# Performance work log

Hardware: AMD Instinct MI355X
Metric: run time of the kernel (lower is better)

The kernel has to match this reference:

```python
import jax, jax.numpy as jnp
import numpy as np

N_NODES = 20000
N_EDGES = 320000
IN_DIM = 128
HID = 256
HEADS = 8
DH = HID // HEADS  # 32
LAYERS = 3
NUM_GRAPHS = 64
OUT_DIM = 10
SLOPE = 0.2  # DGL GATv2Conv default negative_slope


def setup_inputs() -> dict:
    key = jax.random.key(0)
    ks = jax.random.split(key, 20)
    s_in = 1.0 / np.sqrt(IN_DIM)
    s_h = 1.0 / np.sqrt(HID)
    s_h2 = 1.0 / np.sqrt(HID // 2)
    return {
        "feature": jax.random.normal(ks[0], (N_NODES, IN_DIM), jnp.float32),
        "W_in": jax.random.normal(ks[1], (IN_DIM, HID), jnp.float32) * s_in,
        "b_in": jax.random.normal(ks[2], (HID,), jnp.float32) * 0.01,
        "W_src": jax.random.normal(ks[3], (LAYERS, HID, HID), jnp.float32) * s_h,
        "b_src": jax.random.normal(ks[4], (LAYERS, HID), jnp.float32) * 0.01,
        "W_dst": jax.random.normal(ks[5], (LAYERS, HID, HID), jnp.float32) * s_h,
        "b_dst": jax.random.normal(ks[6], (LAYERS, HID), jnp.float32) * 0.01,
        "attn": jax.random.normal(ks[7], (LAYERS, HEADS, DH), jnp.float32) * (1.0 / np.sqrt(DH)),
        "Wc1": jax.random.normal(ks[8], (HID, HID), jnp.float32) * s_h,
        "bc1": jax.random.normal(ks[9], (HID,), jnp.float32) * 0.01,
        "Wc2": jax.random.normal(ks[10], (HID, HID // 2), jnp.float32) * s_h,
        "bc2": jax.random.normal(ks[11], (HID // 2,), jnp.float32) * 0.01,
        "Wc3": jax.random.normal(ks[12], (HID // 2, OUT_DIM), jnp.float32) * s_h2,
        "bc3": jax.random.normal(ks[13], (OUT_DIM,), jnp.float32) * 0.01,
        "src": jax.random.randint(ks[14], (N_EDGES,), 0, N_NODES, jnp.int32),
        "dst": jax.random.randint(ks[15], (N_EDGES,), 0, N_NODES, jnp.int32),
        "graph_ids": jnp.sort(jax.random.randint(ks[16], (N_NODES,), 0, NUM_GRAPHS, jnp.int32)),
    }


def _gatv2_layer(h, Ws, bs, Wd, bd, a, src, dst):
    # DGL GATv2Conv: e_ij = a^T LeakyReLU(W_src h_j + W_dst h_i), edge softmax over
    # incoming edges of dst, scatter-sum of alpha * W_src h_src; residual = Identity
    # (in_feats == heads*out_feats); activation relu.
    n = h.shape[0]
    fs = (h @ Ws + bs).reshape(n, HEADS, DH)  # [N,H,D]
    fd = (h @ Wd + bd).reshape(n, HEADS, DH)
    e = jax.nn.leaky_relu(fs[src] + fd[dst], SLOPE)          # [E,H,D]
    score = jnp.einsum("ehd,hd->eh", e, a)                   # [E,H]
    m = jax.ops.segment_max(score, dst, num_segments=n)       # stable softmax max
    ex = jnp.exp(score - m[dst])
    denom = jax.ops.segment_sum(ex, dst, num_segments=n)
    alpha = ex / denom[dst]                                    # [E,H]
    rst = jax.ops.segment_sum(alpha[:, :, None] * fs[src], dst, num_segments=n)
    out = jax.nn.relu(rst + h.reshape(n, HEADS, DH))          # residual + activation
    return out.reshape(n, HID)


def reference(feature, W_in, b_in, W_src, b_src, W_dst, b_dst, attn,
              Wc1, bc1, Wc2, bc2, Wc3, bc3, src, dst, graph_ids):
    h = feature @ W_in + b_in
    for l in range(LAYERS):
        h = _gatv2_layer(h, W_src[l], b_src[l], W_dst[l], b_dst[l], attn[l], src, dst)
    # dgl.sum_nodes over batched graph -> per-graph segment sum
    hg = jax.ops.segment_sum(h, graph_ids, num_segments=NUM_GRAPHS)  # [G,HID]
    # classifier (dropout is identity in eval mode)
    x = jax.nn.relu(hg @ Wc1 + bc1)
    x = jax.nn.relu(x @ Wc2 + bc2)
    return x @ Wc3 + bc3  # [G,OUT_DIM]
```

## Files before the change

### kernel.cpp

```cpp
#include <hip/hip_runtime.h>
#include <hip/hip_bf16.h>
#include <math.h>

#define N_NODES 20000
#define N_EDGES 320000
#define IN_DIM 128
#define HID 256
#define HEADS 8
#define DH 32
#define LAYERS 3
#define NUM_GRAPHS 64
#define OUT_DIM 10
#define SLOPE 0.2f

#define NBKT 5
#define N_BINS (N_NODES * NBKT)
#define SCAN_BLK 1024
#define SCAN_NBLK ((N_BINS + SCAN_BLK - 1) / SCAN_BLK)

typedef __bf16 bf16x8 __attribute__((ext_vector_type(8)));
typedef float f32x4 __attribute__((ext_vector_type(4)));

static __device__ __forceinline__ unsigned short f2bfbits(float v) {
    __bf16 b = (__bf16)v;
    return __builtin_bit_cast(unsigned short, b);
}
static __device__ __forceinline__ void unpack8(uint4 u, float* f) {
    unsigned p0 = u.x, p1 = u.y, p2 = u.z, p3 = u.w;
    f[0] = __builtin_bit_cast(float, p0 << 16);
    f[1] = __builtin_bit_cast(float, p0 & 0xffff0000u);
    f[2] = __builtin_bit_cast(float, p1 << 16);
    f[3] = __builtin_bit_cast(float, p1 & 0xffff0000u);
    f[4] = __builtin_bit_cast(float, p2 << 16);
    f[5] = __builtin_bit_cast(float, p2 & 0xffff0000u);
    f[6] = __builtin_bit_cast(float, p3 << 16);
    f[7] = __builtin_bit_cast(float, p3 & 0xffff0000u);
}
static __device__ __forceinline__ void unpack4(uint2 u, float* f) {
    f[0] = __builtin_bit_cast(float, u.x << 16);
    f[1] = __builtin_bit_cast(float, u.x & 0xffff0000u);
    f[2] = __builtin_bit_cast(float, u.y << 16);
    f[3] = __builtin_bit_cast(float, u.y & 0xffff0000u);
}

typedef const __attribute__((address_space(1))) unsigned int* as1_u32p;
typedef __attribute__((address_space(3))) unsigned int* as3_u32p;
static __device__ __forceinline__ void async_cp16(const unsigned short* g, unsigned short* l) {
    __builtin_amdgcn_global_load_lds((as1_u32p)g, (as3_u32p)l, 16, 0, 0);
}

#define CAST_N4 (N_NODES * IN_DIM / 4)
#define WTRANS_TOTAL (IN_DIM * HID + 6 * HID * HID)
#define ZERO_TOTAL (N_BINS + NUM_GRAPHS * HID)
#define PREP_TOTAL (CAST_N4 + WTRANS_TOTAL + ZERO_TOTAL)
__global__ void prep_kernel(const float* __restrict__ feat,
                            const float* __restrict__ Win,
                            const float* __restrict__ Wsrc,
                            const float* __restrict__ Wdst,
                            unsigned short* __restrict__ featH,
                            unsigned short* __restrict__ WinT,
                            unsigned short* __restrict__ WT,
                            int* __restrict__ cnt, float* __restrict__ hg) {
    int idx = blockIdx.x * blockDim.x + threadIdx.x;
    if (idx < CAST_N4) {
        float4 v = ((const float4*)feat)[idx];
        ushort4 o;
        o.x = f2bfbits(v.x); o.y = f2bfbits(v.y);
        o.z = f2bfbits(v.z); o.w = f2bfbits(v.w);
        ((ushort4*)featH)[idx] = o;
    } else if (idx < CAST_N4 + WTRANS_TOTAL) {
        int j = idx - CAST_N4;
        if (j < IN_DIM * HID) {
            int n = j / IN_DIM, k = j % IN_DIM;
            WinT[j] = f2bfbits(Win[k * HID + n]);
        } else {
            int r6 = j - IN_DIM * HID;
            int mat = r6 >> 16;
            int r = r6 & 65535;
            int n = r >> 8, k = r & 255;
            const float* base = (mat < 3) ? (Wsrc + (size_t)mat * 65536)
                                          : (Wdst + (size_t)(mat - 3) * 65536);
            WT[r6] = f2bfbits(base[k * 256 + n]);
        }
    } else if (idx < PREP_TOTAL) {
        int z = idx - CAST_N4 - WTRANS_TOTAL;
        if (z < N_BINS) cnt[z] = 0;
        else hg[z - N_BINS] = 0.f;
    }
}

__global__ void count_kernel(const int* __restrict__ src, const int* __restrict__ dst,
                             int* __restrict__ cnt) {
    int e = blockIdx.x * blockDim.x + threadIdx.x;
    if (e < N_EDGES) atomicAdd(&cnt[dst[e] * NBKT + (src[e] >> 12)], 1);
}

__global__ __launch_bounds__(1024) void scan_partial(const int* __restrict__ cnt,
                                                     int* __restrict__ bsum) {
    __shared__ int wsum[16];
    int t = threadIdx.x;
    int idx = blockIdx.x * SCAN_BLK + t;
    int x = (idx < N_BINS) ? cnt[idx] : 0;
    int v = x;
#pragma unroll
    for (int d = 1; d < 64; d <<= 1) v += __shfl_xor(v, d, 64);
    if ((t & 63) == 0) wsum[t >> 6] = v;
    __syncthreads();
    if (t == 0) {
        int s = 0;
#pragma unroll
        for (int i = 0; i < 16; ++i) s += wsum[i];
        bsum[blockIdx.x] = s;
    }
}

__global__ __launch_bounds__(1024) void scan_scatter(const int* __restrict__ cnt,
                                                     const int* __restrict__ bsum,
                                                     int* __restrict__ offs,
                                                     int* __restrict__ cursor) {
    __shared__ int wsum[16];
    __shared__ int bpart[128];
    __shared__ int sbase;
    int t = threadIdx.x;
    int blk = blockIdx.x;
    if (t < 128) bpart[t] = (t < blk) ? bsum[t] : 0;
    __syncthreads();
    if (t < 64) {
        int r = bpart[t] + bpart[t + 64];
#pragma unroll
        for (int d = 1; d < 64; d <<= 1) r += __shfl_xor(r, d, 64);
        if (t == 0) sbase = r;
    }
    int idx = blk * SCAN_BLK + t;
    int x = (idx < N_BINS) ? cnt[idx] : 0;
    int v = x;
#pragma unroll
    for (int d = 1; d < 64; d <<= 1) {
        int u = __shfl_up(v, d, 64);
        if ((t & 63) >= d) v += u;
    }
    if ((t & 63) == 63) wsum[t >> 6] = v;
    __syncthreads();
    if (t < 16) {
        int wv = wsum[t];
#pragma unroll
        for (int d = 1; d < 16; d <<= 1) {
            int u = __shfl_up(wv, d, 64);
            if (t >= d) wv += u;
        }
        wsum[t] = wv;
    }
    __syncthreads();
    int waveoff = (t >> 6) ? wsum[(t >> 6) - 1] : 0;
    int ex = sbase + waveoff + v - x;
    if (idx < N_BINS) { offs[idx] = ex; cursor[idx] = ex; }
    if (blk == SCAN_NBLK - 1 && t == SCAN_BLK - 1) offs[N_BINS] = ex + x;
}

__global__ void fill_kernel(const int* __restrict__ src, const int* __restrict__ dst,
                            int* __restrict__ cursor, int* __restrict__ csr_src) {
    int e = blockIdx.x * blockDim.x + threadIdx.x;
    if (e < N_EDGES) {
        int sv = src[e];
        int p = atomicAdd(&cursor[dst[e] * NBKT + (sv >> 12)], 1);
        csr_src[p] = sv;
    }
}

template <int DUAL>
__global__ __launch_bounds__(256, 4) void mfma_gemm(
    const unsigned short* __restrict__ Ah,
    const unsigned short* __restrict__ BT1, const float* __restrict__ bias1,
    unsigned short* __restrict__ O1,
    const unsigned short* __restrict__ BT2, const float* __restrict__ bias2,
    unsigned short* __restrict__ O2,
    int M, int K, int N) {
    __shared__ __align__(16) unsigned short As[2][64 * 32];
    __shared__ __align__(16) unsigned short Bs1[2][128 * 32];
    __shared__ __align__(16) unsigned short Bs2[DUAL ? 2 : 1][DUAL ? 128 * 32 : 8];

    const int t = threadIdx.x;
    const int wv = t >> 6, lane = t & 63, quad = lane >> 4, l15 = lane & 15;
    const int m0 = blockIdx.x * 64, n0 = blockIdx.y * 128;

    const int sA = wv * 64 + lane;
    const int rA = sA >> 2, cA = (sA & 3) ^ ((rA >> 1) & 3);
    int gmA = m0 + rA; if (gmA >= M) gmA = M - 1;
    const size_t offA = (size_t)gmA * K + cA * 8;
    const int sB0 = wv * 64 + lane, sB1v = sB0 + 256;
    const int rB0 = sB0 >> 2, cB0 = (sB0 & 3) ^ ((rB0 >> 1) & 3);
    const int rB1 = sB1v >> 2, cB1 = (sB1v & 3) ^ ((rB1 >> 1) & 3);
    const size_t offB0 = (size_t)(n0 + rB0) * K + cB0 * 8;
    const size_t offB1 = (size_t)(n0 + rB1) * K + cB1 * 8;

    auto issue = [&](int buf, int k0) {
        async_cp16(Ah + offA + k0, &As[buf][wv * 512]);
        async_cp16(BT1 + offB0 + k0, &Bs1[buf][wv * 512]);
        async_cp16(BT1 + offB1 + k0, &Bs1[buf][2048 + wv * 512]);
        if (DUAL) {
            async_cp16(BT2 + offB0 + k0, &Bs2[buf][wv * 512]);
            async_cp16(BT2 + offB1 + k0, &Bs2[buf][2048 + wv * 512]);
        }
    };

    const int mrow0 = (wv >> 1) * 32;
    const int ncb = (wv & 1) * 64;

    f32x4 zero = {0.f, 0.f, 0.f, 0.f};
    f32x4 acc1[2][4], acc2[2][4];
#pragma unroll
    for (int mi = 0; mi < 2; ++mi)
#pragma unroll
        for (int t4 = 0; t4 < 4; ++t4) { acc1[mi][t4] = zero; acc2[mi][t4] = zero; }

    issue(0, 0);
    int buf = 0;
    for (int k0 = 0; k0 < K; k0 += 32, buf ^= 1) {
        __syncthreads();
        if (k0 + 32 < K) issue(buf ^ 1, k0 + 32);

        bf16x8 aF[2];
#pragma unroll
        for (int mi = 0; mi < 2; ++mi) {
            int row = mrow0 + mi * 16 + l15;
            int aoff = row * 32 + ((quad ^ ((row >> 1) & 3)) << 3);
            aF[mi] = __builtin_bit_cast(bf16x8, *(const uint4*)(&As[buf][0] + aoff));
        }
#pragma unroll
        for (int t4 = 0; t4 < 4; ++t4) {
            int brow = ncb + t4 * 16 + l15;
            int boff = brow * 32 + ((quad ^ ((brow >> 1) & 3)) << 3);
            bf16x8 b1 = __builtin_bit_cast(bf16x8, *(const uint4*)(&Bs1[buf][0] + boff));
#pragma unroll
            for (int mi = 0; mi < 2; ++mi)
                acc1[mi][t4] = __builtin_amdgcn_mfma_f32_16x16x32_bf16(aF[mi], b1, acc1[mi][t4], 0, 0, 0);
            if (DUAL) {
                bf16x8 b2 = __builtin_bit_cast(bf16x8, *(const uint4*)(&Bs2[buf][0] + boff));
#pragma unroll
                for (int mi = 0; mi < 2; ++mi)
                    acc2[mi][t4] = __builtin_amdgcn_mfma_f32_16x16x32_bf16(aF[mi], b2, acc2[mi][t4], 0, 0, 0);
            }
        }
    }

    float bia1[4], bia2[4];
#pragma unroll
    for (int t4 = 0; t4 < 4; ++t4) {
        bia1[t4] = bias1[n0 + ncb + t4 * 16 + l15];
        bia2[t4] = DUAL ? bias2[n0 + ncb + t4 * 16 + l15] : 0.f;
    }
#pragma unroll
    for (int mi = 0; mi < 2; ++mi) {
#pragma unroll
        for (int t4 = 0; t4 < 4; ++t4) {
            int gn = n0 + ncb + t4 * 16 + l15;
#pragma unroll
            for (int r = 0; r < 4; ++r) {
                int gm = m0 + mrow0 + mi * 16 + quad * 4 + r;
                if (gm < M) {
                    float v = acc1[mi][t4][r] + bia1[t4];
                    O1[(size_t)gm * N + gn] = f2bfbits(v);
                    if (DUAL) {
                        float v2 = acc2[mi][t4][r] + bia2[t4];
                        O2[(size_t)gm * N + gn] = f2bfbits(v2);
                    }
                }
            }
        }
    }
}

__global__ __launch_bounds__(256) void gat_agg2(
    const unsigned short* __restrict__ fsb, const unsigned short* __restrict__ fdb,
    unsigned short* __restrict__ hb, const int* __restrict__ offs,
    const int* __restrict__ csr_src, const float* __restrict__ attn_l) {
    int tid = threadIdx.x;
    int node = (blockIdx.x * blockDim.x + tid) >> 5;
    if (node >= N_NODES) return;
    int l32 = tid & 31;
    int dbase = l32 * 8;
    int abase = (l32 >> 2) * DH + (l32 & 3) * 8;

    float a[8];
#pragma unroll
    for (int j = 0; j < 8; ++j) a[j] = attn_l[abase + j];

    float fdv[8];
    unpack8(*(const uint4*)(fdb + (size_t)node * HID + dbase), fdv);

    float ssum0 = 0.f, ssum1 = 0.f;
    float acc0[8], acc1[8];
#pragma unroll
    for (int j = 0; j < 8; ++j) { acc0[j] = 0.f; acc1[j] = 0.f; }

    auto procE = [&](uint4 u, float* acc, float& ssum) {
        float fsv[8];
        unpack8(u, fsv);
        float p = 0.f;
#pragma unroll
        for (int j = 0; j < 8; ++j) {
            float e = fsv[j] + fdv[j];
            e = fmaxf(e, SLOPE * e);
            p += e * a[j];
        }
        p += __shfl_xor(p, 1, 64);
        p += __shfl_xor(p, 2, 64);
        float w = __expf(p);
        ssum += w;
#pragma unroll
        for (int j = 0; j < 8; ++j) acc[j] += w * fsv[j];
    };

    const unsigned short* fsl = fsb + dbase;
    int beg = offs[node * NBKT], end = offs[node * NBKT + NBKT];
    int nfull = (end - beg) >> 2;
    const int limit = beg + nfull * 4;

    uint4 cu0, cu1, cu2, cu3;
    int ci0, ci1, ci2, ci3;
    int base = beg + 8;
    bool have = (nfull >= 1);
    bool haveN = (nfull >= 2);
    if (have) {
        int s0 = csr_src[beg], s1 = csr_src[beg + 1];
        int s2 = csr_src[beg + 2], s3 = csr_src[beg + 3];
        if (haveN) {
            ci0 = csr_src[beg + 4]; ci1 = csr_src[beg + 5];
            ci2 = csr_src[beg + 6]; ci3 = csr_src[beg + 7];
        }
        cu0 = *(const uint4*)(fsl + (size_t)s0 * HID);
        cu1 = *(const uint4*)(fsl + (size_t)s1 * HID);
        cu2 = *(const uint4*)(fsl + (size_t)s2 * HID);
        cu3 = *(const uint4*)(fsl + (size_t)s3 * HID);
    }
    while (have) {
        uint4 nu0, nu1, nu2, nu3;
        int ni0, ni1, ni2, ni3;
        if (haveN) {
            nu0 = *(const uint4*)(fsl + (size_t)ci0 * HID);
            nu1 = *(const uint4*)(fsl + (size_t)ci1 * HID);
            nu2 = *(const uint4*)(fsl + (size_t)ci2 * HID);
            nu3 = *(const uint4*)(fsl + (size_t)ci3 * HID);
        }
        bool haveNN = (base + 4 <= limit);
        if (haveNN) {
            ni0 = csr_src[base]; ni1 = csr_src[base + 1];
            ni2 = csr_src[base + 2]; ni3 = csr_src[base + 3];
        }
        base += 4;
        procE(cu0, acc0, ssum0);
        procE(cu1, acc1, ssum1);
        procE(cu2, acc0, ssum0);
        procE(cu3, acc1, ssum1);
        if (haveN) { cu0 = nu0; cu1 = nu1; cu2 = nu2; cu3 = nu3; }
        if (haveNN) { ci0 = ni0; ci1 = ni1; ci2 = ni2; ci3 = ni3; }
        have = haveN; haveN = haveNN;
    }
    for (int idx = limit; idx < end; ++idx) {
        int sv = csr_src[idx];
        procE(*(const uint4*)(fsl + (size_t)sv * HID), acc0, ssum0);
    }

    float ssum = ssum0 + ssum1;
    float acc[8];
#pragma unroll
    for (int j = 0; j < 8; ++j) acc[j] = acc0[j] + acc1[j];

    float inv = ssum > 0.f ? 1.f / ssum : 0.f;
    float hv[8];
    unpack8(*(const uint4*)(hb + (size_t)node * HID + dbase), hv);
    unsigned short ob[8];
#pragma unroll
    for (int j = 0; j < 8; ++j) {
        float o = fmaxf(acc[j] * inv + hv[j], 0.f);
        ob[j] = f2bfbits(o);
    }
    *(uint4*)(hb + (size_t)node * HID + dbase) = *(uint4*)ob;
}

#define POOL_CHUNK 32
__global__ __launch_bounds__(64) void pool_kernel(const unsigned short* __restrict__ hb,
                                                  const int* __restrict__ gid,
                                                  float* __restrict__ hg) {
    int t = threadIdx.x;
    int n0 = blockIdx.x * POOL_CHUNK;
    int n1 = n0 + POOL_CHUNK; if (n1 > N_NODES) n1 = N_NODES;
    if (n0 >= N_NODES) return;
    float acc[4] = {0.f, 0.f, 0.f, 0.f};
    int cur = gid[n0];
    for (int n = n0; n < n1; ++n) {
        int g = gid[n];
        if (g != cur) {
            atomicAdd(&hg[(size_t)cur * HID + t * 4 + 0], acc[0]);
            atomicAdd(&hg[(size_t)cur * HID + t * 4 + 1], acc[1]);
            atomicAdd(&hg[(size_t)cur * HID + t * 4 + 2], acc[2]);
            atomicAdd(&hg[(size_t)cur * HID + t * 4 + 3], acc[3]);
            acc[0] = acc[1] = acc[2] = acc[3] = 0.f;
            cur = g;
        }
        float v[4];
        unpack4(*(const uint2*)(hb + (size_t)n * HID + t * 4), v);
        acc[0] += v[0]; acc[1] += v[1]; acc[2] += v[2]; acc[3] += v[3];
    }
    atomicAdd(&hg[(size_t)cur * HID + t * 4 + 0], acc[0]);
    atomicAdd(&hg[(size_t)cur * HID + t * 4 + 1], acc[1]);
    atomicAdd(&hg[(size_t)cur * HID + t * 4 + 2], acc[2]);
    atomicAdd(&hg[(size_t)cur * HID + t * 4 + 3], acc[3]);
}

__global__ __launch_bounds__(256) void classifier_kernel(
    const float* __restrict__ hg,
    const float* __restrict__ Wc1, const float* __restrict__ bc1,
    const float* __restrict__ Wc2, const float* __restrict__ bc2,
    const float* __restrict__ Wc3, const float* __restrict__ bc3,
    float* __restrict__ out) {
    __shared__ float xin[HID];
    __shared__ float x1[HID];
    __shared__ float x2[HID / 2];
    int g = blockIdx.x, t = threadIdx.x;
    xin[t] = hg[(size_t)g * HID + t];
    __syncthreads();
    {
        float acc = bc1[t];
        for (int k = 0; k < HID; ++k) acc += xin[k] * Wc1[k * HID + t];
        x1[t] = fmaxf(acc, 0.f);
    }
    __syncthreads();
    if (t < HID / 2) {
        float acc = bc2[t];
        for (int k = 0; k < HID; ++k) acc += x1[k] * Wc2[k * (HID / 2) + t];
        x2[t] = fmaxf(acc, 0.f);
    }
    __syncthreads();
    if (t < OUT_DIM) {
        float acc = bc3[t];
        for (int k = 0; k < HID / 2; ++k) acc += x2[k] * Wc3[k * OUT_DIM + t];
        out[g * OUT_DIM + t] = acc;
    }
}

extern "C" void kernel_launch(void* const* d_in, const int* in_sizes, int n_in,
                              void* d_out, int out_size, void* d_ws, size_t ws_size,
                              hipStream_t stream) {
    const float* feature = (const float*)d_in[0];
    const float* W_in   = (const float*)d_in[1];
    const float* b_in   = (const float*)d_in[2];
    const float* W_src  = (const float*)d_in[3];
    const float* b_src  = (const float*)d_in[4];
    const float* W_dst  = (const float*)d_in[5];
    const float* b_dst  = (const float*)d_in[6];
    const float* attn   = (const float*)d_in[7];
    const float* Wc1    = (const float*)d_in[8];
    const float* bc1    = (const float*)d_in[9];
    const float* Wc2    = (const float*)d_in[10];
    const float* bc2    = (const float*)d_in[11];
    const float* Wc3    = (const float*)d_in[12];
    const float* bc3    = (const float*)d_in[13];
    const int* src     = (const int*)d_in[14];
    const int* dst     = (const int*)d_in[15];
    const int* gid     = (const int*)d_in[16];
    float* out = (float*)d_out;

    char* w = (char*)d_ws;
    auto alloc = [&](size_t bytes) -> void* {
        void* p = (void*)w;
        w += (bytes + 255) & ~(size_t)255;
        return p;
    };
    unsigned short* hb  = (unsigned short*)alloc((size_t)N_NODES * HID * 2);
    unsigned short* fsb = (unsigned short*)alloc((size_t)N_NODES * HID * 2);
    unsigned short* fdb = (unsigned short*)alloc((size_t)N_NODES * HID * 2);
    float* hg    = (float*)alloc((size_t)NUM_GRAPHS * HID * 4);
    int* cnt     = (int*)alloc((size_t)N_BINS * 4);
    int* offs    = (int*)alloc((size_t)(N_BINS + 1) * 4);
    int* cursor  = (int*)alloc((size_t)N_BINS * 4);
    int* csr_src = (int*)alloc((size_t)N_EDGES * 4);
    int* bsum    = (int*)alloc((size_t)SCAN_NBLK * 4);
    unsigned short* WinT = (unsigned short*)alloc((size_t)IN_DIM * HID * 2);
    unsigned short* WT   = (unsigned short*)alloc((size_t)6 * HID * HID * 2);
    unsigned short* featH = (unsigned short*)alloc((size_t)N_NODES * IN_DIM * 2);
    (void)alloc(4096);

    hipLaunchKernelGGL(prep_kernel, dim3((PREP_TOTAL + 255) / 256), dim3(256), 0, stream,
                       feature, W_in, W_src, W_dst, featH, WinT, WT, cnt, hg);

    hipLaunchKernelGGL(count_kernel, dim3((N_EDGES + 255) / 256), dim3(256), 0, stream,
                       src, dst, cnt);
    hipLaunchKernelGGL(scan_partial, dim3(SCAN_NBLK), dim3(SCAN_BLK), 0, stream, cnt, bsum);
    hipLaunchKernelGGL(scan_scatter, dim3(SCAN_NBLK), dim3(SCAN_BLK), 0, stream,
                       cnt, bsum, offs, cursor);
    hipLaunchKernelGGL(fill_kernel, dim3((N_EDGES + 255) / 256), dim3(256), 0, stream,
                       src, dst, cursor, csr_src);

    dim3 ggrid((N_NODES + 63) / 64, HID / 128);

    hipLaunchKernelGGL((mfma_gemm<0>), ggrid, dim3(256), 0, stream,
                       featH, WinT, b_in, hb,
                       (const unsigned short*)nullptr, (const float*)nullptr,
                       (unsigned short*)nullptr,
                       N_NODES, IN_DIM, HID);

    for (int l = 0; l < LAYERS; ++l) {
        hipLaunchKernelGGL((mfma_gemm<1>), ggrid, dim3(256), 0, stream,
                           hb,
                           WT + (size_t)l * HID * HID, b_src + (size_t)l * HID, fsb,
                           WT + (size_t)(3 + l) * HID * HID, b_dst + (size_t)l * HID, fdb,
                           N_NODES, HID, HID);
        hipLaunchKernelGGL(gat_agg2, dim3(N_NODES / 8), dim3(256), 0, stream,
                           fsb, fdb, hb, offs, csr_src, attn + (size_t)l * HEADS * DH);
    }

    hipLaunchKernelGGL(pool_kernel, dim3((N_NODES + POOL_CHUNK - 1) / POOL_CHUNK), dim3(64), 0, stream,
                       hb, gid, hg);
    hipLaunchKernelGGL(classifier_kernel, dim3(NUM_GRAPHS), dim3(256), 0, stream,
                       hg, Wc1, bc1, Wc2, bc2, Wc3, bc3, out);
}
```

Baseline: 313.7 us.

## Fuse whole GAT pipeline into one cooperative persistent kernel with grid syncs

Result: slower. 1.111 ms (+254.3%).

```diff
diff --git a/kernel.cpp b/kernel.cpp
--- a/kernel.cpp
+++ b/kernel.cpp
@@ -1,6 +1,9 @@
 #include <hip/hip_runtime.h>
 #include <hip/hip_bf16.h>
+#include <hip/hip_cooperative_groups.h>
 #include <math.h>
+
+namespace cg = cooperative_groups;
 
 #define N_NODES 20000
 #define N_EDGES 320000
@@ -15,8 +18,12 @@
 
 #define NBKT 5
 #define N_BINS (N_NODES * NBKT)
-#define SCAN_BLK 1024
-#define SCAN_NBLK ((N_BINS + SCAN_BLK - 1) / SCAN_BLK)
+#define N_SCB ((N_BINS + 255) / 256)
+
+#define NT_GEMM 626
+#define NE_CHUNKS 1250
+#define NAGG (N_NODES / 8)
+#define NPOOL ((N_NODES + 31) / 32)
 
 typedef __bf16 bf16x8 __attribute__((ext_vector_type(8)));
 typedef float f32x4 __attribute__((ext_vector_type(4)));
@@ -36,12 +43,6 @@
     f[6] = __builtin_bit_cast(float, p3 << 16);
     f[7] = __builtin_bit_cast(float, p3 & 0xffff0000u);
 }
-static __device__ __forceinline__ void unpack4(uint2 u, float* f) {
-    f[0] = __builtin_bit_cast(float, u.x << 16);
-    f[1] = __builtin_bit_cast(float, u.x & 0xffff0000u);
-    f[2] = __builtin_bit_cast(float, u.y << 16);
-    f[3] = __builtin_bit_cast(float, u.y & 0xffff0000u);
-}
 
 typedef const __attribute__((address_space(1))) unsigned int* as1_u32p;
 typedef __attribute__((address_space(3))) unsigned int* as3_u32p;
@@ -53,15 +54,16 @@
 #define WTRANS_TOTAL (IN_DIM * HID + 6 * HID * HID)
 #define ZERO_TOTAL (N_BINS + NUM_GRAPHS * HID)
 #define PREP_TOTAL (CAST_N4 + WTRANS_TOTAL + ZERO_TOTAL)
-__global__ void prep_kernel(const float* __restrict__ feat,
-                            const float* __restrict__ Win,
-                            const float* __restrict__ Wsrc,
-                            const float* __restrict__ Wdst,
-                            unsigned short* __restrict__ featH,
-                            unsigned short* __restrict__ WinT,
-                            unsigned short* __restrict__ WT,
-                            int* __restrict__ cnt, float* __restrict__ hg) {
-    int idx = blockIdx.x * blockDim.x + threadIdx.x;
+
+static __device__ void prep_item(int idx,
+                                 const float* __restrict__ feat,
+                                 const float* __restrict__ Win,
+                                 const float* __restrict__ Wsrc,
+                                 const float* __restrict__ Wdst,
+                                 unsigned short* __restrict__ featH,
+                                 unsigned short* __restrict__ WinT,
+                                 unsigned short* __restrict__ WT,
+                                 int* __restrict__ cnt, float* __restrict__ hg) {
     if (idx < CAST_N4) {
         float4 v = ((const float4*)feat)[idx];
         ushort4 o;
@@ -89,99 +91,63 @@
     }
 }
 
-__global__ void count_kernel(const int* __restrict__ src, const int* __restrict__ dst,
-                             int* __restrict__ cnt) {
-    int e = blockIdx.x * blockDim.x + threadIdx.x;
-    if (e < N_EDGES) atomicAdd(&cnt[dst[e] * NBKT + (src[e] >> 12)], 1);
-}
-
-__global__ __launch_bounds__(1024) void scan_partial(const int* __restrict__ cnt,
-                                                     int* __restrict__ bsum) {
-    __shared__ int wsum[16];
-    int t = threadIdx.x;
-    int idx = blockIdx.x * SCAN_BLK + t;
+static __device__ void scanp_unit(int u, int t, const int* __restrict__ cnt,
+                                  int* __restrict__ bsum, int* si) {
+    int idx = u * 256 + t;
+    int x = (idx < N_BINS) ? cnt[idx] : 0;
+#pragma unroll
+    for (int d = 1; d < 64; d <<= 1) x += __shfl_xor(x, d, 64);
+    if ((t & 63) == 0) si[t >> 6] = x;
+    __syncthreads();
+    if (t == 0) bsum[u] = si[0] + si[1] + si[2] + si[3];
+    __syncthreads();
+}
+
+static __device__ void scans_unit(int u, int t, const int* __restrict__ cnt,
+                                  const int* __restrict__ bsum, int* __restrict__ offs,
+                                  int* __restrict__ cursor, int* si) {
+    int bv = 0;
+    if (t < u) bv = bsum[t];
+    if (t + 256 < u) bv += bsum[t + 256];
+#pragma unroll
+    for (int d = 1; d < 64; d <<= 1) bv += __shfl_xor(bv, d, 64);
+    if ((t & 63) == 0) si[t >> 6] = bv;
+    __syncthreads();
+    int sbase = si[0] + si[1] + si[2] + si[3];
+    __syncthreads();
+    int idx = u * 256 + t;
     int x = (idx < N_BINS) ? cnt[idx] : 0;
     int v = x;
 #pragma unroll
-    for (int d = 1; d < 64; d <<= 1) v += __shfl_xor(v, d, 64);
-    if ((t & 63) == 0) wsum[t >> 6] = v;
-    __syncthreads();
-    if (t == 0) {
-        int s = 0;
-#pragma unroll
-        for (int i = 0; i < 16; ++i) s += wsum[i];
-        bsum[blockIdx.x] = s;
-    }
-}
-
-__global__ __launch_bounds__(1024) void scan_scatter(const int* __restrict__ cnt,
-                                                     const int* __restrict__ bsum,
-                                                     int* __restrict__ offs,
-                                                     int* __restrict__ cursor) {
-    __shared__ int wsum[16];
-    __shared__ int bpart[128];
-    __shared__ int sbase;
-    int t = threadIdx.x;
-    int blk = blockIdx.x;
-    if (t < 128) bpart[t] = (t < blk) ? bsum[t] : 0;
-    __syncthreads();
-    if (t < 64) {
-        int r = bpart[t] + bpart[t + 64];
-#pragma unroll
-        for (int d = 1; d < 64; d <<= 1) r += __shfl_xor(r, d, 64);
-        if (t == 0) sbase = r;
-    }
-    int idx = blk * SCAN_BLK + t;
-    int x = (idx < N_BINS) ? cnt[idx] : 0;
-    int v = x;
-#pragma unroll
     for (int d = 1; d < 64; d <<= 1) {
-        int u = __shfl_up(v, d, 64);
-        if ((t & 63) >= d) v += u;
-    }
-    if ((t & 63) == 63) wsum[t >> 6] = v;
-    __syncthreads();
-    if (t < 16) {
-        int wv = wsum[t];
-#pragma unroll
-        for (int d = 1; d < 16; d <<= 1) {
-            int u = __shfl_up(wv, d, 64);
-            if (t >= d) wv += u;
-        }
-        wsum[t] = wv;
-    }
-    __syncthreads();
-    int waveoff = (t >> 6) ? wsum[(t >> 6) - 1] : 0;
-    int ex = sbase + waveoff + v - x;
+        int w = __shfl_up(v, d, 64);
+        if ((t & 63) >= d) v += w;
+    }
+    if ((t & 63) == 63) si[t >> 6] = v;
+    __syncthreads();
+    int woff = 0;
+#pragma unroll
+    for (int w2 = 0; w2 < 4; ++w2) if (w2 < (t >> 6)) woff += si[w2];
+    int ex = sbase + woff + v - x;
     if (idx < N_BINS) { offs[idx] = ex; cursor[idx] = ex; }
-    if (blk == SCAN_NBLK - 1 && t == SCAN_BLK - 1) offs[N_BINS] = ex + x;
-}
-
-__global__ void fill_kernel(const int* __restrict__ src, const int* __restrict__ dst,
-                            int* __restrict__ cursor, int* __restrict__ csr_src) {
-    int e = blockIdx.x * blockDim.x + threadIdx.x;
-    if (e < N_EDGES) {
-        int sv = src[e];
-        int p = atomicAdd(&cursor[dst[e] * NBKT + (sv >> 12)], 1);
-        csr_src[p] = sv;
-    }
+    if (u == N_SCB - 1 && t == 255) offs[N_BINS] = ex + x;
+    __syncthreads();
 }
 
 template <int DUAL>
-__global__ __launch_bounds__(256, 4) void mfma_gemm(
-    const unsigned short* __restrict__ Ah,
-    const unsigned short* __restrict__ BT1, const float* __restrict__ bias1,
-    unsigned short* __restrict__ O1,
-    const unsigned short* __restrict__ BT2, const float* __restrict__ bias2,
-    unsigned short* __restrict__ O2,
-    int M, int K, int N) {
-    __shared__ __align__(16) unsigned short As[2][64 * 32];
-    __shared__ __align__(16) unsigned short Bs1[2][128 * 32];
-    __shared__ __align__(16) unsigned short Bs2[DUAL ? 2 : 1][DUAL ? 128 * 32 : 8];
-
-    const int t = threadIdx.x;
+static __device__ void gemm_tile(int mt, int nt, int t,
+                                 const unsigned short* __restrict__ Ah,
+                                 const unsigned short* __restrict__ BT1,
+                                 const float* __restrict__ bias1,
+                                 unsigned short* __restrict__ O1,
+                                 const unsigned short* __restrict__ BT2,
+                                 const float* __restrict__ bias2,
+                                 unsigned short* __restrict__ O2,
+                                 int M, int K, int N,
+                                 unsigned short* AsP, unsigned short* Bs1P,
+                                 unsigned short* Bs2P) {
     const int wv = t >> 6, lane = t & 63, quad = lane >> 4, l15 = lane & 15;
-    const int m0 = blockIdx.x * 64, n0 = blockIdx.y * 128;
+    const int m0 = mt * 64, n0 = nt * 128;
 
     const int sA = wv * 64 + lane;
     const int rA = sA >> 2, cA = (sA & 3) ^ ((rA >> 1) & 3);
@@ -194,12 +160,12 @@
     const size_t offB1 = (size_t)(n0 + rB1) * K + cB1 * 8;
 
     auto issue = [&](int buf, int k0) {
-        async_cp16(Ah + offA + k0, &As[buf][wv * 512]);
-        async_cp16(BT1 + offB0 + k0, &Bs1[buf][wv * 512]);
-        async_cp16(BT1 + offB1 + k0, &Bs1[buf][2048 + wv * 512]);
+        async_cp16(Ah + offA + k0, AsP + buf * 2048 + wv * 512);
+        async_cp16(BT1 + offB0 + k0, Bs1P + buf * 4096 + wv * 512);
+        async_cp16(BT1 + offB1 + k0, Bs1P + buf * 4096 + 2048 + wv * 512);
         if (DUAL) {
-            async_cp16(BT2 + offB0 + k0, &Bs2[buf][wv * 512]);
-            async_cp16(BT2 + offB1 + k0, &Bs2[buf][2048 + wv * 512]);
+            async_cp16(BT2 + offB0 + k0, Bs2P + buf * 4096 + wv * 512);
+            async_cp16(BT2 + offB1 + k0, Bs2P + buf * 4096 + 2048 + wv * 512);
         }
     };
 
@@ -224,18 +190,18 @@
         for (int mi = 0; mi < 2; ++mi) {
             int row = mrow0 + mi * 16 + l15;
             int aoff = row * 32 + ((quad ^ ((row >> 1) & 3)) << 3);
-            aF[mi] = __builtin_bit_cast(bf16x8, *(const uint4*)(&As[buf][0] + aoff));
+            aF[mi] = __builtin_bit_cast(bf16x8, *(const uint4*)(AsP + buf * 2048 + aoff));
         }
 #pragma unroll
         for (int t4 = 0; t4 < 4; ++t4) {
             int brow = ncb + t4 * 16 + l15;
             int boff = brow * 32 + ((quad ^ ((brow >> 1) & 3)) << 3);
-            bf16x8 b1 = __builtin_bit_cast(bf16x8, *(const uint4*)(&Bs1[buf][0] + boff));
+            bf16x8 b1 = __builtin_bit_cast(bf16x8, *(const uint4*)(Bs1P + buf * 4096 + boff));
 #pragma unroll
             for (int mi = 0; mi < 2; ++mi)
                 acc1[mi][t4] = __builtin_amdgcn_mfma_f32_16x16x32_bf16(aF[mi], b1, acc1[mi][t4], 0, 0, 0);
             if (DUAL) {
-                bf16x8 b2 = __builtin_bit_cast(bf16x8, *(const uint4*)(&Bs2[buf][0] + boff));
+                bf16x8 b2 = __builtin_bit_cast(bf16x8, *(const uint4*)(Bs2P + buf * 4096 + boff));
 #pragma unroll
                 for (int mi = 0; mi < 2; ++mi)
                     acc2[mi][t4] = __builtin_amdgcn_mfma_f32_16x16x32_bf16(aF[mi], b2, acc2[mi][t4], 0, 0, 0);
@@ -270,14 +236,16 @@
     }
 }
 
-__global__ __launch_bounds__(256) void gat_agg2(
-    const unsigned short* __restrict__ fsb, const unsigned short* __restrict__ fdb,
-    unsigned short* __restrict__ hb, const int* __restrict__ offs,
-    const int* __restrict__ csr_src, const float* __restrict__ attn_l) {
-    int tid = threadIdx.x;
-    int node = (blockIdx.x * blockDim.x + tid) >> 5;
+static __device__ void agg_unit(int u, int t,
+                                const unsigned short* __restrict__ fsb,
+                                const unsigned short* __restrict__ fdb,
+                                unsigned short* __restrict__ hb,
+                                const int* __restrict__ offs,
+                                const int* __restrict__ csr_src,
+                                const float* __restrict__ attn_l) {
+    int node = u * 8 + (t >> 5);
     if (node >= N_NODES) return;
-    int l32 = tid & 31;
+    int l32 = t & 31;
     int dbase = l32 * 8;
     int abase = (l32 >> 2) * DH + (l32 & 3) * 8;
 
@@ -293,9 +261,9 @@
 #pragma unroll
     for (int j = 0; j < 8; ++j) { acc0[j] = 0.f; acc1[j] = 0.f; }
 
-    auto procE = [&](uint4 u, float* acc, float& ssum) {
+    auto procE = [&](uint4 uu, float* acc, float& ssum) {
         float fsv[8];
-        unpack8(u, fsv);
+        unpack8(uu, fsv);
         float p = 0.f;
 #pragma unroll
         for (int j = 0; j < 8; ++j) {
@@ -378,46 +346,34 @@
     *(uint4*)(hb + (size_t)node * HID + dbase) = *(uint4*)ob;
 }
 
-#define POOL_CHUNK 32
-__global__ __launch_bounds__(64) void pool_kernel(const unsigned short* __restrict__ hb,
-                                                  const int* __restrict__ gid,
-                                                  float* __restrict__ hg) {
-    int t = threadIdx.x;
-    int n0 = blockIdx.x * POOL_CHUNK;
-    int n1 = n0 + POOL_CHUNK; if (n1 > N_NODES) n1 = N_NODES;
+static __device__ void pool_unit(int u, int t, const unsigned short* __restrict__ hb,
+                                 const int* __restrict__ gid, float* __restrict__ hg) {
+    int n0 = u * 32;
+    int n1 = n0 + 32; if (n1 > N_NODES) n1 = N_NODES;
     if (n0 >= N_NODES) return;
-    float acc[4] = {0.f, 0.f, 0.f, 0.f};
+    float acc = 0.f;
     int cur = gid[n0];
     for (int n = n0; n < n1; ++n) {
         int g = gid[n];
         if (g != cur) {
-            atomicAdd(&hg[(size_t)cur * HID + t * 4 + 0], acc[0]);
-            atomicAdd(&hg[(size_t)cur * HID + t * 4 + 1], acc[1]);
-            atomicAdd(&hg[(size_t)cur * HID + t * 4 + 2], acc[2]);
-            atomicAdd(&hg[(size_t)cur * HID + t * 4 + 3], acc[3]);
-            acc[0] = acc[1] = acc[2] = acc[3] = 0.f;
+            atomicAdd(&hg[(size_t)cur * HID + t], acc);
+            acc = 0.f;
             cur = g;
         }
-        float v[4];
-        unpack4(*(const uint2*)(hb + (size_t)n * HID + t * 4), v);
-        acc[0] += v[0]; acc[1] += v[1]; acc[2] += v[2]; acc[3] += v[3];
-    }
-    atomicAdd(&hg[(size_t)cur * HID + t * 4 + 0], acc[0]);
-    atomicAdd(&hg[(size_t)cur * HID + t * 4 + 1], acc[1]);
-    atomicAdd(&hg[(size_t)cur * HID + t * 4 + 2], acc[2]);
-    atomicAdd(&hg[(size_t)cur * HID + t * 4 + 3], acc[3]);
-}
-
-__global__ __launch_bounds__(256) void classifier_kernel(
-    const float* __restrict__ hg,
-    const float* __restrict__ Wc1, const float* __restrict__ bc1,
-    const float* __restrict__ Wc2, const float* __restrict__ bc2,
-    const float* __restrict__ Wc3, const float* __restrict__ bc3,
-    float* __restrict__ out) {
-    __shared__ float xin[HID];
-    __shared__ float x1[HID];
-    __shared__ float x2[HID / 2];
-    int g = blockIdx.x, t = threadIdx.x;
+        unsigned v = hb[(size_t)n * HID + t];
+        acc += __builtin_bit_cast(float, v << 16);
+    }
+    atomicAdd(&hg[(size_t)cur * HID + t], acc);
+}
+
+static __device__ void cls_unit(int g, int t, float* sf, const float* __restrict__ hg,
+                                const float* __restrict__ Wc1, const float* __restrict__ bc1,
+                                const float* __restrict__ Wc2, const float* __restrict__ bc2,
+                                const float* __restrict__ Wc3, const float* __restrict__ bc3,
+                                float* __restrict__ out) {
+    float* xin = sf;
+    float* x1 = sf + HID;
+    float* x2 = sf + 2 * HID;
     xin[t] = hg[(size_t)g * HID + t];
     __syncthreads();
     {
@@ -437,6 +393,151 @@
         for (int k = 0; k < HID / 2; ++k) acc += x2[k] * Wc3[k * OUT_DIM + t];
         out[g * OUT_DIM + t] = acc;
     }
+    __syncthreads();
+}
+
+struct MegaParams {
+    const float* feature; const float* W_in; const float* b_in;
+    const float* W_src; const float* b_src; const float* W_dst; const float* b_dst;
+    const float* attn;
+    const float* Wc1; const float* bc1; const float* Wc2; const float* bc2;
+    const float* Wc3; const float* bc3;
+    const int* src; const int* dst; const int* gid;
+    float* out;
+    unsigned short* hb; unsigned short* fsb; unsigned short* fdb;
+    float* hg; int* cnt; int* offs; int* cursor; int* csr_src; int* bsum;
+    unsigned short* WinT; unsigned short* WT; unsigned short* featH;
+};
+
+__global__ __launch_bounds__(256, 4) void mega_kernel(MegaParams P) {
+    cg::grid_group gg = cg::this_grid();
+    __shared__ __align__(16) unsigned short smem[20480];
+    unsigned short* AsP  = smem;
+    unsigned short* Bs1P = smem + 4096;
+    unsigned short* Bs2P = smem + 12288;
+    int* si = (int*)(void*)smem;
+    float* sf = (float*)(void*)smem;
+
+    const int t = threadIdx.x;
+    const int bid = blockIdx.x;
+    const int nblk = gridDim.x;
+
+    for (int idx = bid * 256 + t; idx < PREP_TOTAL; idx += nblk * 256)
+        prep_item(idx, P.feature, P.W_in, P.W_src, P.W_dst, P.featH, P.WinT, P.WT, P.cnt, P.hg);
+    gg.sync();
+
+    for (int u = bid; u < NT_GEMM + NE_CHUNKS; u += nblk) {
+        if (u < NT_GEMM)
+            gemm_tile<0>(u >> 1, u & 1, t, P.featH, P.WinT, P.b_in, P.hb,
+                         (const unsigned short*)nullptr, (const float*)nullptr,
+                         (unsigned short*)nullptr, N_NODES, IN_DIM, HID, AsP, Bs1P, Bs2P);
+        else {
+            int e = (u - NT_GEMM) * 256 + t;
+            if (e < N_EDGES) atomicAdd(&P.cnt[P.dst[e] * NBKT + (P.src[e] >> 12)], 1);
+        }
+    }
+    gg.sync();
+
+    for (int u = bid; u < N_SCB + NT_GEMM; u += nblk) {
+        if (u < N_SCB) scanp_unit(u, t, P.cnt, P.bsum, si);
+        else {
+            int g = u - N_SCB;
+            gemm_tile<1>(g >> 1, g & 1, t, P.hb, P.WT, P.b_src, P.fsb,
+                         P.WT + 3 * 65536, P.b_dst, P.fdb, N_NODES, HID, HID, AsP, Bs1P, Bs2P);
+        }
+    }
+    gg.sync();
+
+    for (int u = bid; u < N_SCB; u += nblk)
+        scans_unit(u, t, P.cnt, P.bsum, P.offs, P.cursor, si);
+    gg.sync();
+
+    for (int u = bid; u < NE_CHUNKS; u += nblk) {
+        int e = u * 256 + t;
+        if (e < N_EDGES) {
+            int sv = P.src[e];
+            int p = atomicAdd(&P.cursor[P.dst[e] * NBKT + (sv >> 12)], 1);
+            P.csr_src[p] = sv;
+        }
+    }
+    gg.sync();
+
+    for (int l = 0; l < LAYERS; ++l) {
+        for (int u = bid; u < NAGG; u += nblk)
+            agg_unit(u, t, P.fsb, P.fdb, P.hb, P.offs, P.csr_src,
+                     P.attn + (size_t)l * HEADS * DH);
+        gg.sync();
+        if (l + 1 < LAYERS) {
+            for (int u = bid; u < NT_GEMM; u += nblk)
+                gemm_tile<1>(u >> 1, u & 1, t, P.hb,
+                             P.WT + (size_t)(l + 1) * 65536, P.b_src + (l + 1) * HID, P.fsb,
+                             P.WT + (size_t)(4 + l) * 65536, P.b_dst + (l + 1) * HID, P.fdb,
+                             N_NODES, HID, HID, AsP, Bs1P, Bs2P);
+            gg.sync();
+        }
+    }
+
+    for (int u = bid; u < NPOOL; u += nblk)
+        pool_unit(u, t, P.hb, P.gid, P.hg);
+    gg.sync();
+
+    for (int u = bid; u < NUM_GRAPHS; u += nblk)
+        cls_unit(u, t, sf, P.hg, P.Wc1, P.bc1, P.Wc2, P.bc2, P.Wc3, P.bc3, P.out);
+}
+
+__global__ void prep_kernel(const float* feat, const float* Win, const float* Wsrc,
+                            const float* Wdst, unsigned short* featH, unsigned short* WinT,
+                            unsigned short* WT, int* cnt, float* hg) {
+    prep_item(blockIdx.x * blockDim.x + threadIdx.x, feat, Win, Wsrc, Wdst,
+              featH, WinT, WT, cnt, hg);
+}
+__global__ void count_kernel(const int* src, const int* dst, int* cnt) {
+    int e = blockIdx.x * blockDim.x + threadIdx.x;
+    if (e < N_EDGES) atomicAdd(&cnt[dst[e] * NBKT + (src[e] >> 12)], 1);
+}
+__global__ __launch_bounds__(256) void scanp_kernel(const int* cnt, int* bsum) {
+    __shared__ int si[4];
+    scanp_unit(blockIdx.x, threadIdx.x, cnt, bsum, si);
+}
+__global__ __launch_bounds__(256) void scans_kernel(const int* cnt, const int* bsum,
+                                                    int* offs, int* cursor) {
+    __shared__ int si[4];
+    scans_unit(blockIdx.x, threadIdx.x, cnt, bsum, offs, cursor, si);
+}
+__global__ void fill_kernel(const int* src, const int* dst, int* cursor, int* csr_src) {
+    int e = blockIdx.x * blockDim.x + threadIdx.x;
+    if (e < N_EDGES) {
+        int sv = src[e];
+        int p = atomicAdd(&cursor[dst[e] * NBKT + (sv >> 12)], 1);
+        csr_src[p] = sv;
+    }
+}
+template <int DUAL>
+__global__ __launch_bounds__(256, 4) void gemm_kernel(
+    const unsigned short* Ah, const unsigned short* BT1, const float* bias1,
+    unsigned short* O1, const unsigned short* BT2, const float* bias2,
+    unsigned short* O2, int M, int K, int N) {
+    __shared__ __align__(16) unsigned short smem[20480];
+    gemm_tile<DUAL>(blockIdx.x, blockIdx.y, threadIdx.x, Ah, BT1, bias1, O1,
+                    BT2, bias2, O2, M, K, N, smem, smem + 4096, smem + 12288);
+}
+__global__ __launch_bounds__(256) void agg_kernel(const unsigned short* fsb,
+                                                  const unsigned short* fdb,
+                                                  unsigned short* hb, const int* offs,
+                                                  const int* csr_src, const float* attn_l) {
+    agg_unit(blockIdx.x, threadIdx.x, fsb, fdb, hb, offs, csr_src, attn_l);
+}
+__global__ __launch_bounds__(256) void pool_kernel(const unsigned short* hb, const int* gid,
+                                                   float* hg) {
+    pool_unit(blockIdx.x, threadIdx.x, hb, gid, hg);
+}
+__global__ __launch_bounds__(256) void cls_kernel(const float* hg,
+                                                  const float* Wc1, const float* bc1,
+                                                  const float* Wc2, const float* bc2,
+                                                  const float* Wc3, const float* bc3,
+                                                  float* out) {
+    __shared__ float sf[HID * 2 + HID / 2];
+    cls_unit(blockIdx.x, threadIdx.x, sf, hg, Wc1, bc1, Wc2, bc2, Wc3, bc3, out);
 }
 
 extern "C" void kernel_launch(void* const* d_in, const int* in_sizes, int n_in,
@@ -475,43 +576,73 @@
     int* offs    = (int*)alloc((size_t)(N_BINS + 1) * 4);
     int* cursor  = (int*)alloc((size_t)N_BINS * 4);
     int* csr_src = (int*)alloc((size_t)N_EDGES * 4);
-    int* bsum    = (int*)alloc((size_t)SCAN_NBLK * 4);
+    int* bsum    = (int*)alloc((size_t)N_SCB * 4);
     unsigned short* WinT = (unsigned short*)alloc((size_t)IN_DIM * HID * 2);
     unsigned short* WT   = (unsigned short*)alloc((size_t)6 * HID * HID * 2);
     unsigned short* featH = (unsigned short*)alloc((size_t)N_NODES * IN_DIM * 2);
     (void)alloc(4096);
 
+    MegaParams mp;
+    mp.feature = feature; mp.W_in = W_in; mp.b_in = b_in;
+    mp.W_src = W_src; mp.b_src = b_src; mp.W_dst = W_dst; mp.b_dst = b_dst;
+    mp.attn = attn;
+    mp.Wc1 = Wc1; mp.bc1 = bc1; mp.Wc2 = Wc2; mp.bc2 = bc2; mp.Wc3 = Wc3; mp.bc3 = bc3;
+    mp.src = src; mp.dst = dst; mp.gid = gid;
+    mp.out = out;
+    mp.hb = hb; mp.fsb = fsb; mp.fdb = fdb;
+    mp.hg = hg; mp.cnt = cnt; mp.offs = offs; mp.cursor = cursor; mp.csr_src = csr_src;
+    mp.bsum = bsum; mp.WinT = WinT; mp.WT = WT; mp.featH = featH;
+
+    static int coop_grid = -2;
+    if (coop_grid == -2) {
+        int dev = 0; (void)hipGetDevice(&dev);
+        int sup = 0;
+        (void)hipDeviceGetAttribute(&sup, hipDeviceAttributeCooperativeLaunch, dev);
+        int ncu = 0;
+        (void)hipDeviceGetAttribute(&ncu, hipDeviceAttributeMultiprocessorCount, dev);
+        int nb = 0;
+        if (sup && ncu >= 1 &&
+            hipOccupancyMaxActiveBlocksPerMultiprocessor(&nb, mega_kernel, 256, 0) == hipSuccess &&
+            nb >= 1) {
+            long g = (long)nb * (long)ncu;
+            if (g > 1024) g = 1024;
+            coop_grid = (int)g;
+        } else {
+            coop_grid = -1;
+        }
+    }
+
+    if (coop_grid > 0) {
+        void* kargs[] = { (void*)&mp };
+        hipError_t err = hipLaunchCooperativeKernel(mega_kernel, dim3(coop_grid), dim3(256),
+                                                    kargs, 0, stream);
+        if (err == hipSuccess) return;
+        coop_grid = -1;
+    }
+
     hipLaunchKernelGGL(prep_kernel, dim3((PREP_TOTAL + 255) / 256), dim3(256), 0, stream,
                        feature, W_in, W_src, W_dst, featH, WinT, WT, cnt, hg);
-
     hipLaunchKernelGGL(count_kernel, dim3((N_EDGES + 255) / 256), dim3(256), 0, stream,
                        src, dst, cnt);
-    hipLaunchKernelGGL(scan_partial, dim3(SCAN_NBLK), dim3(SCAN_BLK), 0, stream, cnt, bsum);
-    hipLaunchKernelGGL(scan_scatter, dim3(SCAN_NBLK), dim3(SCAN_BLK), 0, stream,
-                       cnt, bsum, offs, cursor);
+    hipLaunchKernelGGL(scanp_kernel, dim3(N_SCB), dim3(256), 0, stream, cnt, bsum);
+    hipLaunchKernelGGL(scans_kernel, dim3(N_SCB), dim3(256), 0, stream, cnt, bsum, offs, cursor);
     hipLaunchKernelGGL(fill_kernel, dim3((N_EDGES + 255) / 256), dim3(256), 0, stream,
                        src, dst, cursor, csr_src);
 
-    dim3 ggrid((N_NODES + 63) / 64, HID / 128);
-
-    hipLaunchKernelGGL((mfma_gemm<0>), ggrid, dim3(256), 0, stream,
+    dim3 ggrid(313, 2);
+    hipLaunchKernelGGL((gemm_kernel<0>), ggrid, dim3(256), 0, stream,
                        featH, WinT, b_in, hb,
                        (const unsigned short*)nullptr, (const float*)nullptr,
-                       (unsigned short*)nullptr,
-                       N_NODES, IN_DIM, HID);
-
+                       (unsigned short*)nullptr, N_NODES, IN_DIM, HID);
     for (int l = 0; l < LAYERS; ++l) {
-        hipLaunchKernelGGL((mfma_gemm<1>), ggrid, dim3(256), 0, stream,
-                           hb,
-                           WT + (size_t)l * HID * HID, b_src + (size_t)l * HID, fsb,
+        hipLaunchKernelGGL((gemm_kernel<1>), ggrid, dim3(256), 0, stream,
+                           hb, WT + (size_t)l * HID * HID, b_src + (size_t)l * HID, fsb,
                            WT + (size_t)(3 + l) * HID * HID, b_dst + (size_t)l * HID, fdb,
                            N_NODES, HID, HID);
-        hipLaunchKernelGGL(gat_agg2, dim3(N_NODES / 8), dim3(256), 0, stream,
+        hipLaunchKernelGGL(agg_kernel, dim3(NAGG), dim3(256), 0, stream,
                            fsb, fdb, hb, offs, csr_src, attn + (size_t)l * HEADS * DH);
     }
-
-    hipLaunchKernelGGL(pool_kernel, dim3((N_NODES + POOL_CHUNK - 1) / POOL_CHUNK), dim3(64), 0, stream,
-                       hb, gid, hg);
-    hipLaunchKernelGGL(classifier_kernel, dim3(NUM_GRAPHS), dim3(256), 0, stream,
+    hipLaunchKernelGGL(pool_kernel, dim3(NPOOL), dim3(256), 0, stream, hb, gid, hg);
+    hipLaunchKernelGGL(cls_kernel, dim3(NUM_GRAPHS), dim3(256), 0, stream,
                        hg, Wc1, bc1, Wc2, bc2, Wc3, bc3, out);
 }
```
